# Performance work log

Measured on AMD Instinct MI355X. Metric: run time of the kernel, lower is better.

## Reference

```python
import jax, jax.numpy as jnp
import numpy as np

N = 30000      # particles
E = 300000     # directed edges
H = 128        # hidden size
L = 10         # GNN layers
EMB = 16       # particle-type embedding size
T = 5          # velocity history window
NTYPES = 9
RADIUS = 0.05
OUT = 2
NODE_IN = 2 * T + 4 + EMB  # 30


def _mlp_ln(x, W1, b1, W2, b2, W3, b3, g, be):
    # Linear-ReLU-Linear-ReLU-Linear-LayerNorm (matches node/edge encoders and GraphNet blocks)
    h = jax.nn.relu(x @ W1 + b1)
    h = jax.nn.relu(h @ W2 + b2)
    h = h @ W3 + b3
    mu = jnp.mean(h, axis=-1, keepdims=True)
    var = jnp.mean((h - mu) ** 2, axis=-1, keepdims=True)
    return (h - mu) * jax.lax.rsqrt(var + 1e-5) * g + be


def setup_inputs() -> dict:
    key = jax.random.key(0)
    ks = iter(jax.random.split(key, 48))
    nx = lambda: next(ks)
    inp = {}
    inp["vel"] = jax.random.normal(nx(), (N, T, 2), jnp.float32) * 0.01
    inp["pos"] = jax.random.uniform(nx(), (N, 2), dtype=jnp.float32)
    inp["bounds"] = jnp.array([[0.0, 1.0], [0.0, 1.0]], jnp.float32)  # [dim, (lo,hi)]
    inp["tgt_pos"] = jax.random.uniform(nx(), (N, 2), dtype=jnp.float32)
    inp["particle_type"] = jax.random.randint(nx(), (N,), 0, NTYPES, jnp.int32)
    inp["nonk_mask"] = jax.random.randint(nx(), (N,), 0, 2, jnp.int32)
    inp["senders"] = jax.random.randint(nx(), (E,), 0, N, jnp.int32)
    inp["receivers"] = jax.random.randint(nx(), (E,), 0, N, jnp.int32)
    inp["emb"] = jax.random.normal(nx(), (NTYPES, EMB), jnp.float32) * 0.1

    def mlp_p(pre, din, lead=()):
        w = lambda i, o: jax.random.normal(nx(), lead + (i, o), jnp.float32) / np.sqrt(i)
        inp[pre + "_W1"] = w(din, H); inp[pre + "_b1"] = jnp.zeros(lead + (H,), jnp.float32)
        inp[pre + "_W2"] = w(H, H);   inp[pre + "_b2"] = jnp.zeros(lead + (H,), jnp.float32)
        inp[pre + "_W3"] = w(H, H);   inp[pre + "_b3"] = jnp.zeros(lead + (H,), jnp.float32)
        inp[pre + "_g"] = jnp.ones(lead + (H,), jnp.float32)
        inp[pre + "_be"] = jnp.zeros(lead + (H,), jnp.float32)

    mlp_p("ne", NODE_IN)          # node encoder
    mlp_p("ee", 3)                # edge encoder
    mlp_p("ge", 3 * H, (L,))      # per-layer edge-update MLPs
    mlp_p("gn", 2 * H, (L,))      # per-layer node-update MLPs
    inp["de_W1"] = jax.random.normal(nx(), (H, H), jnp.float32) / np.sqrt(H)
    inp["de_b1"] = jnp.zeros((H,), jnp.float32)
    inp["de_W2"] = jax.random.normal(nx(), (H, H), jnp.float32) / np.sqrt(H)
    inp["de_b2"] = jnp.zeros((H,), jnp.float32)
    inp["de_W3"] = jax.random.normal(nx(), (H, OUT), jnp.float32) / np.sqrt(H)
    inp["de_b3"] = jnp.zeros((OUT,), jnp.float32)
    return inp


def reference(vel, pos, bounds, tgt_pos, particle_type, nonk_mask, senders, receivers, emb,
              ne_W1, ne_b1, ne_W2, ne_b2, ne_W3, ne_b3, ne_g, ne_be,
              ee_W1, ee_b1, ee_W2, ee_b2, ee_W3, ee_b3, ee_g, ee_be,
              ge_W1, ge_b1, ge_W2, ge_b2, ge_W3, ge_b3, ge_g, ge_be,
              gn_W1, gn_b1, gn_W2, gn_b2, gn_W3, gn_b3, gn_g, gn_be,
              de_W1, de_b1, de_W2, de_b2, de_W3, de_b3):
    n = pos.shape[0]
    # --- construct node features ---
    vels = vel.reshape(n, -1)                                   # [N, T*2]
    dtw = jnp.concatenate([pos - bounds[:, 0], bounds[:, 1] - pos], axis=1)
    dtw = jnp.clip(dtw / RADIUS, -1.0, 1.0)                     # [N, 4]
    type_emb = emb[particle_type]                               # [N, EMB] gather
    node_attr = jnp.concatenate([vels, dtw, type_emb], axis=1)  # [N, 30]
    # --- construct edge features (senders/receivers precomputed; KD-tree is CPU-side) ---
    dist_vec = (pos[senders] - pos[receivers]) / RADIUS         # [E, 2]
    dist = jnp.linalg.norm(dist_vec, axis=1, keepdims=True)     # [E, 1]
    edge_attr = jnp.concatenate([dist_vec, dist], axis=1)       # [E, 3]
    # --- encode ---
    nodes = _mlp_ln(node_attr, ne_W1, ne_b1, ne_W2, ne_b2, ne_W3, ne_b3, ne_g, ne_be)
    edges = _mlp_ln(edge_attr, ee_W1, ee_b1, ee_W2, ee_b2, ee_W3, ee_b3, ee_g, ee_be)
    # --- process: L message-passing layers with residuals ---
    for l in range(ge_W1.shape[0]):
        e_in = jnp.concatenate([edges, nodes[senders], nodes[receivers]], axis=1)  # [E, 3H]
        edges = edges + _mlp_ln(e_in, ge_W1[l], ge_b1[l], ge_W2[l], ge_b2[l], ge_W3[l], ge_b3[l], ge_g[l], ge_be[l])
        agg = jax.ops.segment_sum(edges, receivers, num_segments=n)               # [N, H] scatter-add
        n_in = jnp.concatenate([nodes, agg], axis=1)                              # [N, 2H]
        nodes = nodes + _mlp_ln(n_in, gn_W1[l], gn_b1[l], gn_W2[l], gn_b2[l], gn_W3[l], gn_b3[l], gn_g[l], gn_be[l])
    # --- decode ---
    h = jax.nn.relu(nodes @ de_W1 + de_b1)
    h = jax.nn.relu(h @ de_W2 + de_b2)
    pred_acc = h @ de_W3 + de_b3                                 # [N, 2]
    # --- Euler integration step (out_size == 2 branch) ---
    pred_pos = pos + vel[:, -1, :] + pred_acc
    pred_pos = jnp.where(nonk_mask[:, None].astype(bool), pred_pos, tgt_pos)
    return pred_acc[:, None, :], pred_pos[:, None, :]
```

## Files before the change

kernel.cpp:

```cpp
#include <hip/hip_runtime.h>
#include <hip/hip_bf16.h>

typedef __hip_bfloat16 bf16;
typedef unsigned short u16;
typedef unsigned int u32;
typedef __attribute__((ext_vector_type(8))) short short8;
typedef __attribute__((ext_vector_type(4))) float f32x4;
typedef __attribute__((ext_vector_type(4))) unsigned int u32x4;

#define NPART 30000
#define NEDGE 300000
#define HD 128
#define NLAYER 10
#define NFLOAT_ARRAYS 43
#define NMAT 66

__device__ __forceinline__ bool detect_bf16(const unsigned short* braw) {
    return braw[1] == 0x3F80u;
}

__device__ __forceinline__ u16 f2b(float f) {
    u32 u = __float_as_uint(f);
    u += 0x7FFFu + ((u >> 16) & 1u);
    return (u16)(u >> 16);
}
__device__ __forceinline__ u32 pack2(float a, float b) {
    return (u32)f2b(a) | ((u32)f2b(b) << 16);
}
__device__ __forceinline__ float b2flo(u32 u) { return __uint_as_float(u << 16); }
__device__ __forceinline__ float b2fhi(u32 u) { return __uint_as_float(u & 0xFFFF0000u); }

__device__ __forceinline__ u32x4 ntl4(const u16* p) {
    return __builtin_nontemporal_load((const u32x4*)p);
}
__device__ __forceinline__ void nts4(const u32x4 v, u16* p) {
    __builtin_nontemporal_store(v, (u32x4*)p);
}
__device__ __forceinline__ f32x4 ntlf4(const float* p) {
    return __builtin_nontemporal_load((const f32x4*)p);
}
__device__ __forceinline__ void ntsf4(const f32x4 v, float* p) {
    __builtin_nontemporal_store(v, (f32x4*)p);
}

struct ConvArgs {
    const void* src[NFLOAT_ARRAYS];
    int n[NFLOAT_ARRAYS];
    int off[NFLOAT_ARRAYS];
};

__global__ __launch_bounds__(256)
void k_convert(ConvArgs a, float* __restrict__ dst, const unsigned short* __restrict__ braw)
{
    const bool isb = detect_bf16(braw);
    const int aid = blockIdx.y;
    const int n = a.n[aid];
    float* o = dst + a.off[aid];
    const int stride = gridDim.x * 256;
    int i = blockIdx.x * 256 + threadIdx.x;
    if (isb) {
        const unsigned short* s = (const unsigned short*)a.src[aid];
        for (; i < n; i += stride) {
            const unsigned int u = ((unsigned int)s[i]) << 16;
            o[i] = __uint_as_float(u);
        }
    } else {
        const float* s = (const float*)a.src[aid];
        for (; i < n; i += stride) o[i] = s[i];
    }
}

__global__ __launch_bounds__(256)
void k_hist(const int* __restrict__ rcv, int* __restrict__ counts)
{
    const int e = blockIdx.x * 256 + threadIdx.x;
    if (e < NEDGE) atomicAdd(&counts[rcv[e]], 1);
}

__global__ __launch_bounds__(1024)
void k_scan(const int* __restrict__ counts, int* __restrict__ row_ptr, int* __restrict__ cursor)
{
    __shared__ int part[1024];
    const int t = threadIdx.x;
    const int base = t * 32;
    int local[32];
    int s = 0;
#pragma unroll
    for (int k = 0; k < 32; k++) {
        const int idx = base + k;
        const int v = (idx < NPART) ? counts[idx] : 0;
        local[k] = s;
        s += v;
    }
    part[t] = s;
    __syncthreads();
    for (int off = 1; off < 1024; off <<= 1) {
        const int v = (t >= off) ? part[t - off] : 0;
        __syncthreads();
        part[t] += v;
        __syncthreads();
    }
    const int excl = (t == 0) ? 0 : part[t - 1];
#pragma unroll
    for (int k = 0; k < 32; k++) {
        const int idx = base + k;
        if (idx < NPART) {
            const int rp = excl + local[k];
            row_ptr[idx] = rp;
            cursor[idx] = rp;
        }
    }
    if (t == 0) row_ptr[NPART] = NEDGE;
}

__global__ __launch_bounds__(256)
void k_scatter(const int* __restrict__ snd, const int* __restrict__ rcv,
               int* __restrict__ cursor, int* __restrict__ snd_s, int* __restrict__ rcv_s)
{
    const int e = blockIdx.x * 256 + threadIdx.x;
    if (e < NEDGE) {
        const int r = rcv[e];
        const int p = atomicAdd(&cursor[r], 1);
        snd_s[p] = snd[e];
        rcv_s[p] = r;
    }
}

struct PackArgs {
    int src_off[NMAT];
    int dst_off[NMAT];
    int K[NMAT];
    int nks[NMAT];
};

__global__ __launch_bounds__(256)
void k_pack(const float* __restrict__ cw, u16* __restrict__ wpk, PackArgs pa)
{
    const int mid = blockIdx.y;
    const int nks = pa.nks[mid];
    const int total = nks * 4096;
    const int d = blockIdx.x * 256 + threadIdx.x;
    if (d >= total) return;
    const int j = d & 7, l = (d >> 3) & 63, t = d >> 9;
    const int ks = t % nks, mt = t / nks;
    const int hid = mt * 16 + (l & 15);
    const int k = ks * 32 + (l >> 4) * 8 + j;
    const float v = (k < pa.K[mid]) ? cw[pa.src_off[mid] + k * HD + hid] : 0.0f;
    wpk[pa.dst_off[mid] + d] = f2b(v);
}

template<int NKS, int XROW>
__device__ __forceinline__ void gemm16(const u16* __restrict__ Wp,
                                       const float* __restrict__ Bias,
                                       const u16* __restrict__ x,
                                       f32x4 acc[4][2],
                                       const int wm, const int wn,
                                       const int l15, const int lg, const int lane)
{
#pragma unroll
    for (int mt = 0; mt < 4; mt++) {
        const f32x4 bv = *(const f32x4*)(Bias + wm * 64 + mt * 16 + lg * 4);
        acc[mt][0] = bv;
        acc[mt][1] = bv;
    }
    const u16* xr0 = x + (wn * 32 + l15) * XROW + lg * 8;
    const u16* xr1 = xr0 + 16 * XROW;
    const u16* wp = Wp + (wm * 4 * NKS) * 512 + lane * 8;
#pragma unroll
    for (int ks = 0; ks < NKS; ks++) {
        const short8 b0 = *(const short8*)(xr0 + ks * 32);
        const short8 b1 = *(const short8*)(xr1 + ks * 32);
#pragma unroll
        for (int mt = 0; mt < 4; mt++) {
            const short8 a = *(const short8*)(wp + (mt * NKS + ks) * 512);
            acc[mt][0] = __builtin_amdgcn_mfma_f32_16x16x32_bf16(a, b0, acc[mt][0], 0, 0, 0);
            acc[mt][1] = __builtin_amdgcn_mfma_f32_16x16x32_bf16(a, b1, acc[mt][1], 0, 0, 0);
        }
    }
}

__device__ __forceinline__ void store_h(u16* __restrict__ h, const f32x4 acc[4][2],
                                        const int wm, const int wn, const int l15, const int lg)
{
#pragma unroll
    for (int nt = 0; nt < 2; nt++) {
        const int e = wn * 32 + nt * 16 + l15;
#pragma unroll
        for (int mt = 0; mt < 4; mt++) {
            const int hid = wm * 64 + mt * 16 + lg * 4;
            const f32x4 v = acc[mt][nt];
            const u32 lo = pack2(fmaxf(v[0], 0.0f), fmaxf(v[1], 0.0f));
            const u32 hi = pack2(fmaxf(v[2], 0.0f), fmaxf(v[3], 0.0f));
            *(uint2*)(h + e * 136 + hid) = make_uint2(lo, hi);
        }
    }
}

template<int NKS1, int XROW>
__device__ __forceinline__ void mlp_mfma(const u16* __restrict__ xs,
    u16* __restrict__ h1, u16* __restrict__ h2,
    float (*red)[2][2][16][2],
    const u16* __restrict__ W1p, const float* __restrict__ B1,
    const u16* __restrict__ W2p, const float* __restrict__ B2,
    const u16* __restrict__ W3p, const float* __restrict__ B3,
    const float* __restrict__ g, const float* __restrict__ be,
    float outv[4][2][4],
    const int wm, const int wn, const int l15, const int lg, const int lane)
{
    f32x4 acc[4][2];
    gemm16<NKS1, XROW>(W1p, B1, xs, acc, wm, wn, l15, lg, lane);
    __syncthreads();
    store_h(h1, acc, wm, wn, l15, lg);
    __syncthreads();
    gemm16<4, 136>(W2p, B2, h1, acc, wm, wn, l15, lg, lane);
    store_h(h2, acc, wm, wn, l15, lg);
    __syncthreads();
    gemm16<4, 136>(W3p, B3, h2, acc, wm, wn, l15, lg, lane);
    float ps[2], pss[2];
#pragma unroll
    for (int nt = 0; nt < 2; nt++) {
        float s = 0.0f, ss = 0.0f;
#pragma unroll
        for (int mt = 0; mt < 4; mt++) {
#pragma unroll
            for (int r = 0; r < 4; r++) {
                const float v = acc[mt][nt][r];
                s += v; ss += v * v;
            }
        }
        s += __shfl_xor(s, 16); ss += __shfl_xor(ss, 16);
        s += __shfl_xor(s, 32); ss += __shfl_xor(ss, 32);
        ps[nt] = s; pss[nt] = ss;
    }
    if (lane < 16) {
#pragma unroll
        for (int nt = 0; nt < 2; nt++) {
            red[wm][wn][nt][l15][0] = ps[nt];
            red[wm][wn][nt][l15][1] = pss[nt];
        }
    }
    __syncthreads();
#pragma unroll
    for (int nt = 0; nt < 2; nt++) {
        const float S  = red[0][wn][nt][l15][0] + red[1][wn][nt][l15][0];
        const float SS = red[0][wn][nt][l15][1] + red[1][wn][nt][l15][1];
        const float mu  = S * (1.0f / 128.0f);
        const float var = SS * (1.0f / 128.0f) - mu * mu;
        const float inv = rsqrtf(var + 1e-5f);
#pragma unroll
        for (int mt = 0; mt < 4; mt++) {
            const int hid = wm * 64 + mt * 16 + lg * 4;
            const f32x4 gv  = *(const f32x4*)(g + hid);
            const f32x4 bev = *(const f32x4*)(be + hid);
#pragma unroll
            for (int r = 0; r < 4; r++)
                outv[mt][nt][r] = (acc[mt][nt][r] - mu) * inv * gv[r] + bev[r];
        }
    }
}

__device__ __forceinline__ float nfeat(int i, int k,
    const float* __restrict__ vel, const float* __restrict__ pos,
    const float* __restrict__ bounds, const int* __restrict__ ptype,
    const float* __restrict__ emb)
{
    if (k < 10) return vel[i * 10 + k];
    if (k < 14) {
        const int q = k - 10;
        float sub;
        if (q < 2) sub = pos[i * 2 + q] - bounds[q * 2 + 0];
        else       sub = bounds[(q - 2) * 2 + 1] - pos[i * 2 + (q - 2)];
        const float dv = sub * 20.0f;
        return fminf(fmaxf(dv, -1.0f), 1.0f);
    }
    if (k < 30) return emb[ptype[i] * 16 + (k - 14)];
    return 0.0f;
}

__global__ __launch_bounds__(256)
void k_node_enc_m(const float* __restrict__ vel, const float* __restrict__ pos,
                  const float* __restrict__ bounds, const int* __restrict__ ptype,
                  const float* __restrict__ emb,
                  const u16* __restrict__ W1p, const float* __restrict__ B1,
                  const u16* __restrict__ W2p, const float* __restrict__ B2,
                  const u16* __restrict__ W3p, const float* __restrict__ B3,
                  const float* __restrict__ g, const float* __restrict__ be,
                  u16* __restrict__ nodes_bf)
{
    __shared__ __align__(16) u16 lds[17408];
    __shared__ float red[2][2][2][16][2];
    const int tid = threadIdx.x;
    const int i0 = blockIdx.x * 64;
    for (int idx = tid; idx < 1024; idx += 256) {
        const int m = idx >> 4, kk = idx & 15;
        const int i = i0 + m;
        float f0 = 0.0f, f1 = 0.0f;
        if (i < NPART) {
            f0 = nfeat(i, kk * 2 + 0, vel, pos, bounds, ptype, emb);
            f1 = nfeat(i, kk * 2 + 1, vel, pos, bounds, ptype, emb);
        }
        *(u32*)(lds + m * 40 + kk * 2) = pack2(f0, f1);
    }
    __syncthreads();
    const int lane = tid & 63, wv = tid >> 6;
    const int wm = wv >> 1, wn = wv & 1, l15 = lane & 15, lg = lane >> 4;
    float outv[4][2][4];
    mlp_mfma<1, 40>(lds, lds, lds + 8704, red, W1p, B1, W2p, B2, W3p, B3, g, be,
                    outv, wm, wn, l15, lg, lane);
#pragma unroll
    for (int nt = 0; nt < 2; nt++) {
        const int i = i0 + wn * 32 + nt * 16 + l15;
        if (i < NPART) {
#pragma unroll
            for (int mt = 0; mt < 4; mt++) {
                const int hid = wm * 64 + mt * 16 + lg * 4;
                *(uint2*)(nodes_bf + (size_t)i * HD + hid) =
                    make_uint2(pack2(outv[mt][nt][0], outv[mt][nt][1]),
                               pack2(outv[mt][nt][2], outv[mt][nt][3]));
            }
        }
    }
}

__global__ __launch_bounds__(256)
void k_edge_enc_m(const float* __restrict__ pos, const int* __restrict__ snd_s,
                  const int* __restrict__ rcv_s,
                  const u16* __restrict__ W1p, const float* __restrict__ B1,
                  const u16* __restrict__ W2p, const float* __restrict__ B2,
                  const u16* __restrict__ W3p, const float* __restrict__ B3,
                  const float* __restrict__ g, const float* __restrict__ be,
                  u16* __restrict__ edges_bf)
{
    __shared__ __align__(16) u16 lds[17408];
    __shared__ float red[2][2][2][16][2];
    const int tid = threadIdx.x;
    const int e0 = blockIdx.x * 64;
    for (int idx = tid; idx < 1024; idx += 256) {
        const int m = idx >> 4, kk = idx & 15;
        const int e = min(e0 + m, NEDGE - 1);
        u32 w = 0;
        if (kk < 2) {
            const int s = snd_s[e], r = rcv_s[e];
            const float dx = (pos[s * 2 + 0] - pos[r * 2 + 0]) * 20.0f;
            const float dy = (pos[s * 2 + 1] - pos[r * 2 + 1]) * 20.0f;
            if (kk == 0) w = pack2(dx, dy);
            else         w = pack2(sqrtf(dx * dx + dy * dy), 0.0f);
        }
        *(u32*)(lds + m * 40 + kk * 2) = w;
    }
    __syncthreads();
    const int lane = tid & 63, wv = tid >> 6;
    const int wm = wv >> 1, wn = wv & 1, l15 = lane & 15, lg = lane >> 4;
    float outv[4][2][4];
    mlp_mfma<1, 40>(lds, lds, lds + 8704, red, W1p, B1, W2p, B2, W3p, B3, g, be,
                    outv, wm, wn, l15, lg, lane);
#pragma unroll
    for (int nt = 0; nt < 2; nt++) {
        const int e = e0 + wn * 32 + nt * 16 + l15;
        if (e < NEDGE) {
#pragma unroll
            for (int mt = 0; mt < 4; mt++) {
                const int hid = wm * 64 + mt * 16 + lg * 4;
                *(uint2*)(edges_bf + (size_t)e * HD + hid) =
                    make_uint2(pack2(outv[mt][nt][0], outv[mt][nt][1]),
                               pack2(outv[mt][nt][2], outv[mt][nt][3]));
            }
        }
    }
}

__device__ __forceinline__ void egemm_seg32(const u16* __restrict__ Wp,
                                            const u16* __restrict__ x,
                                            f32x4 acc[2][2], const int ks0,
                                            const int wm,
                                            const int l15, const int lg, const int lane)
{
    const u16* xr0 = x + l15 * 136 + lg * 8;
    const u16* xr1 = xr0 + 16 * 136;
#pragma unroll
    for (int ks = 0; ks < 4; ks++) {
        const short8 b0 = *(const short8*)(xr0 + ks * 32);
        const short8 b1 = *(const short8*)(xr1 + ks * 32);
#pragma unroll
        for (int mt = 0; mt < 2; mt++) {
            const short8 a = *(const short8*)(Wp + (((wm * 2 + mt) * 12 + ks0 + ks) * 64 + lane) * 8);
            acc[mt][0] = __builtin_amdgcn_mfma_f32_16x16x32_bf16(a, b0, acc[mt][0], 0, 0, 0);
            acc[mt][1] = __builtin_amdgcn_mfma_f32_16x16x32_bf16(a, b1, acc[mt][1], 0, 0, 0);
        }
    }
}

__device__ __forceinline__ void egemm_h32(const u16* __restrict__ Wp,
                                          const float* __restrict__ Bias,
                                          const u16* __restrict__ x,
                                          f32x4 acc[2][2],
                                          const int wm,
                                          const int l15, const int lg, const int lane)
{
#pragma unroll
    for (int mt = 0; mt < 2; mt++) {
        const f32x4 bv = *(const f32x4*)(Bias + wm * 32 + mt * 16 + lg * 4);
        acc[mt][0] = bv;
        acc[mt][1] = bv;
    }
    const u16* xr0 = x + l15 * 136 + lg * 8;
    const u16* xr1 = xr0 + 16 * 136;
#pragma unroll
    for (int ks = 0; ks < 4; ks++) {
        const short8 b0 = *(const short8*)(xr0 + ks * 32);
        const short8 b1 = *(const short8*)(xr1 + ks * 32);
#pragma unroll
        for (int mt = 0; mt < 2; mt++) {
            const short8 a = *(const short8*)(Wp + (((wm * 2 + mt) * 4 + ks) * 64 + lane) * 8);
            acc[mt][0] = __builtin_amdgcn_mfma_f32_16x16x32_bf16(a, b0, acc[mt][0], 0, 0, 0);
            acc[mt][1] = __builtin_amdgcn_mfma_f32_16x16x32_bf16(a, b1, acc[mt][1], 0, 0, 0);
        }
    }
}

__device__ __forceinline__ void estore_h32(u16* __restrict__ h, const f32x4 acc[2][2],
                                           const int wm, const int l15, const int lg)
{
#pragma unroll
    for (int nt = 0; nt < 2; nt++) {
        const int row = nt * 16 + l15;
#pragma unroll
        for (int mt = 0; mt < 2; mt++) {
            const int hid = wm * 32 + mt * 16 + lg * 4;
            const f32x4 v = acc[mt][nt];
            const u32 lo = pack2(fmaxf(v[0], 0.0f), fmaxf(v[1], 0.0f));
            const u32 hi = pack2(fmaxf(v[2], 0.0f), fmaxf(v[3], 0.0f));
            *(uint2*)(h + row * 136 + hid) = make_uint2(lo, hi);
        }
    }
}

__global__ __launch_bounds__(256, 8)
void k_edge_layer_m(const u16* __restrict__ nodes_bf, u16* __restrict__ edges_bf,
                    float* __restrict__ agg, float* __restrict__ bnd,
                    const int* __restrict__ snd_s, const int* __restrict__ rcv_s,
                    const u16* __restrict__ W1p, const float* __restrict__ B1,
                    const u16* __restrict__ W2p, const float* __restrict__ B2,
                    const u16* __restrict__ W3p, const float* __restrict__ B3,
                    const float* __restrict__ g, const float* __restrict__ be)
{
    __shared__ __align__(16) u16 sb[2 * 4352];
    __shared__ float red[4][2][16][2];
    __shared__ int rblk[34];
    u16* b0 = sb;
    u16* b1 = sb + 4352;
    float* fout = (float*)sb;

    const int tid = threadIdx.x;
    const int e0 = blockIdx.x * 32;
    const int lane = tid & 63, wm = tid >> 6;
    const int l15 = lane & 15, lg = lane >> 4;

    if (tid < 32)       rblk[tid] = rcv_s[e0 + tid];
    else if (tid == 32) rblk[32] = (e0 > 0) ? rcv_s[e0 - 1] : -2;
    else if (tid == 33) rblk[33] = (e0 + 32 < NEDGE) ? rcv_s[e0 + 32] : -2;

    u32x4 e_old[2];
#pragma unroll
    for (int t = 0; t < 2; t++) {
        const int idx = tid + t * 256;
        const int m = idx >> 4, q = idx & 15;
        e_old[t] = ntl4(edges_bf + (size_t)(e0 + m) * HD + q * 8);
        *(u32x4*)(b0 + m * 136 + q * 8) = e_old[t];
    }
    u32x4 st[2];
#pragma unroll
    for (int t = 0; t < 2; t++) {
        const int idx = tid + t * 256;
        const int m = idx >> 4, q = idx & 15;
        st[t] = *(const u32x4*)(nodes_bf + (size_t)snd_s[e0 + m] * HD + q * 8);
    }
    __syncthreads();

    f32x4 acc[2][2];
#pragma unroll
    for (int mt = 0; mt < 2; mt++) {
        const f32x4 bv = *(const f32x4*)(B1 + wm * 32 + mt * 16 + lg * 4);
        acc[mt][0] = bv;
        acc[mt][1] = bv;
    }
    __builtin_amdgcn_s_setprio(1);
    egemm_seg32(W1p, b0, acc, 0, wm, l15, lg, lane);
    __builtin_amdgcn_s_setprio(0);
#pragma unroll
    for (int t = 0; t < 2; t++) {
        const int idx = tid + t * 256;
        const int m = idx >> 4, q = idx & 15;
        *(u32x4*)(b1 + m * 136 + q * 8) = st[t];
    }
#pragma unroll
    for (int t = 0; t < 2; t++) {
        const int idx = tid + t * 256;
        const int m = idx >> 4, q = idx & 15;
        st[t] = *(const u32x4*)(nodes_bf + (size_t)rcv_s[e0 + m] * HD + q * 8);
    }
    __syncthreads();

    __builtin_amdgcn_s_setprio(1);
    egemm_seg32(W1p, b1, acc, 4, wm, l15, lg, lane);
    __builtin_amdgcn_s_setprio(0);
#pragma unroll
    for (int t = 0; t < 2; t++) {
        const int idx = tid + t * 256;
        const int m = idx >> 4, q = idx & 15;
        *(u32x4*)(b0 + m * 136 + q * 8) = st[t];
    }
    __syncthreads();

    __builtin_amdgcn_s_setprio(1);
    egemm_seg32(W1p, b0, acc, 8, wm, l15, lg, lane);
    __builtin_amdgcn_s_setprio(0);
    estore_h32(b1, acc, wm, l15, lg);
    __syncthreads();

    __builtin_amdgcn_s_setprio(1);
    egemm_h32(W2p, B2, b1, acc, wm, l15, lg, lane);
    __builtin_amdgcn_s_setprio(0);
    estore_h32(b0, acc, wm, l15, lg);
    __syncthreads();

    __builtin_amdgcn_s_setprio(1);
    egemm_h32(W3p, B3, b0, acc, wm, l15, lg, lane);
    __builtin_amdgcn_s_setprio(0);

    float ps[2], pss[2];
#pragma unroll
    for (int nt = 0; nt < 2; nt++) {
        float s = 0.0f, ss = 0.0f;
#pragma unroll
        for (int mt = 0; mt < 2; mt++) {
#pragma unroll
            for (int r = 0; r < 4; r++) {
                const float v = acc[mt][nt][r];
                s += v; ss += v * v;
            }
        }
        s += __shfl_xor(s, 16); ss += __shfl_xor(ss, 16);
        s += __shfl_xor(s, 32); ss += __shfl_xor(ss, 32);
        ps[nt] = s; pss[nt] = ss;
    }
    if (lane < 16) {
#pragma unroll
        for (int nt = 0; nt < 2; nt++) {
            red[wm][nt][l15][0] = ps[nt];
            red[wm][nt][l15][1] = pss[nt];
        }
    }
    __syncthreads();

#pragma unroll
    for (int nt = 0; nt < 2; nt++) {
        const float S  = red[0][nt][l15][0] + red[1][nt][l15][0]
                       + red[2][nt][l15][0] + red[3][nt][l15][0];
        const float SS = red[0][nt][l15][1] + red[1][nt][l15][1]
                       + red[2][nt][l15][1] + red[3][nt][l15][1];
        const float mu  = S * (1.0f / 128.0f);
        const float var = SS * (1.0f / 128.0f) - mu * mu;
        const float inv = rsqrtf(var + 1e-5f);
        const int row = nt * 16 + l15;
#pragma unroll
        for (int mt = 0; mt < 2; mt++) {
            const int hid = wm * 32 + mt * 16 + lg * 4;
            const f32x4 gv  = *(const f32x4*)(g + hid);
            const f32x4 bev = *(const f32x4*)(be + hid);
            f32x4 o;
#pragma unroll
            for (int r = 0; r < 4; r++)
                o[r] = (acc[mt][nt][r] - mu) * inv * gv[r] + bev[r];
            *(f32x4*)(fout + row * 132 + hid) = o;
        }
    }
    __syncthreads();

#pragma unroll
    for (int t = 0; t < 2; t++) {
        const int idx = tid + t * 256;
        const int m = idx >> 4, q = idx & 15;
        float4 lo = *(const float4*)(fout + m * 132 + q * 8);
        float4 hi = *(const float4*)(fout + m * 132 + q * 8 + 4);
        const u32x4 o = e_old[t];
        lo.x += b2flo(o.x); lo.y += b2fhi(o.x);
        lo.z += b2flo(o.y); lo.w += b2fhi(o.y);
        hi.x += b2flo(o.z); hi.y += b2fhi(o.z);
        hi.z += b2flo(o.w); hi.w += b2fhi(o.w);
        *(float4*)(fout + m * 132 + q * 8) = lo;
        *(float4*)(fout + m * 132 + q * 8 + 4) = hi;
        u32x4 nv;
        nv.x = pack2(lo.x, lo.y); nv.y = pack2(lo.z, lo.w);
        nv.z = pack2(hi.x, hi.y); nv.w = pack2(hi.z, hi.w);
        nts4(nv, edges_bf + (size_t)(e0 + m) * HD + q * 8);
    }
    __syncthreads();

    const int c = tid & 31;
    for (int ms = (tid >> 5); ms < 32; ms += 8) {
        const int rs = rblk[ms];
        if (ms > 0 && rblk[ms - 1] == rs) continue;
        int me = ms + 1;
        while (me < 32 && rblk[me] == rs) me++;
        f32x4 s = {0.0f, 0.0f, 0.0f, 0.0f};
        for (int m = ms; m < me; m++) {
            const float4 v = *(const float4*)(fout + m * 132 + c * 4);
            s.x += v.x; s.y += v.y; s.z += v.z; s.w += v.w;
        }
        const bool extb = (ms == 0 && rblk[32] == rs);
        const bool extf = (me == 32 && rblk[33] == rs);
        float* ap;
        if (!extb && !extf) ap = agg + (size_t)rs * HD + c * 4;
        else ap = bnd + ((size_t)blockIdx.x * 2 + (extb ? 0 : 1)) * HD + c * 4;
        ntsf4(s, ap);
    }
}

__global__ __launch_bounds__(256)
void k_node_layer_m(u16* __restrict__ nodes_bf,
                    const float* __restrict__ agg, const float* __restrict__ bnd,
                    const int* __restrict__ row_ptr,
                    const u16* __restrict__ W1p, const float* __restrict__ B1,
                    const u16* __restrict__ W2p, const float* __restrict__ B2,
                    const u16* __restrict__ W3p, const float* __restrict__ B3,
                    const float* __restrict__ g, const float* __restrict__ be)
{
    __shared__ __align__(16) u16 lds[17408];
    __shared__ float red[2][2][2][16][2];
    __shared__ int rp[65];
    const int tid = threadIdx.x;
    const int i0 = blockIdx.x * 64;
    if (tid < 65) rp[tid] = row_ptr[min(i0 + tid, NPART)];
    __syncthreads();
    for (int idx = tid; idx < 1024; idx += 256) {
        const int m = idx >> 4, q = idx & 15;
        const int i = min(i0 + m, NPART - 1);
        *(u32x4*)(lds + m * 264 + q * 8) =
            *(const u32x4*)(nodes_bf + (size_t)i * HD + q * 8);
    }
    for (int idx = tid; idx < 1024; idx += 256) {
        const int m = idx >> 4, q = idx & 15;
        const int i = i0 + m;
        f32x4 a = {0.0f, 0.0f, 0.0f, 0.0f};
        f32x4 b = {0.0f, 0.0f, 0.0f, 0.0f};
        if (i < NPART) {
            const int p0 = rp[m], p1 = rp[m + 1];
            if (p1 > p0) {
                const int b0 = p0 >> 5, b1 = (p1 - 1) >> 5;
                if (b0 == b1) {
                    const float* src = agg + (size_t)i * HD + q * 8;
                    a = ntlf4(src);
                    b = ntlf4(src + 4);
                } else {
                    const float* s1 = bnd + ((size_t)b0 * 2 + 1) * HD + q * 8;
                    a = ntlf4(s1);
                    b = ntlf4(s1 + 4);
                    for (int bb = b0 + 1; bb <= b1; bb++) {
                        const float* s0 = bnd + ((size_t)bb * 2 + 0) * HD + q * 8;
                        const f32x4 xa = ntlf4(s0);
                        const f32x4 xb = ntlf4(s0 + 4);
                        a += xa;
                        b += xb;
                    }
                }
            }
        }
        *(u32x4*)(lds + m * 264 + 128 + q * 8) = (u32x4){
            pack2(a.x, a.y), pack2(a.z, a.w), pack2(b.x, b.y), pack2(b.z, b.w)};
    }
    __syncthreads();
    const int lane = tid & 63, wv = tid >> 6;
    const int wm = wv >> 1, wn = wv & 1, l15 = lane & 15, lg = lane >> 4;
    float outv[4][2][4];
    mlp_mfma<8, 264>(lds, lds, lds + 8704, red, W1p, B1, W2p, B2, W3p, B3, g, be,
                     outv, wm, wn, l15, lg, lane);
#pragma unroll
    for (int nt = 0; nt < 2; nt++) {
        const int i = i0 + wn * 32 + nt * 16 + l15;
        if (i < NPART) {
            u16* np = nodes_bf + (size_t)i * HD;
#pragma unroll
            for (int mt = 0; mt < 4; mt++) {
                const int hid = wm * 64 + mt * 16 + lg * 4;
                const uint2 ob = *(const uint2*)(np + hid);
                float4 nv;
                nv.x = b2flo(ob.x) + outv[mt][nt][0];
                nv.y = b2fhi(ob.x) + outv[mt][nt][1];
                nv.z = b2flo(ob.y) + outv[mt][nt][2];
                nv.w = b2fhi(ob.y) + outv[mt][nt][3];
                *(uint2*)(np + hid) = make_uint2(pack2(nv.x, nv.y), pack2(nv.z, nv.w));
            }
        }
    }
}

template<int K, int S>
__device__ __forceinline__ void gemv(const float* __restrict__ in,
                                     const float* __restrict__ W,
                                     const float* __restrict__ B,
                                     float acc[8])
{
    const int j = threadIdx.x;
    const float bb = B[j];
#pragma unroll
    for (int m = 0; m < 8; m++) acc[m] = bb;
    constexpr int K4 = (K / 4) * 4;
    for (int k = 0; k < K4; k += 4) {
        const float w0 = W[(k + 0) * HD + j];
        const float w1 = W[(k + 1) * HD + j];
        const float w2 = W[(k + 2) * HD + j];
        const float w3 = W[(k + 3) * HD + j];
#pragma unroll
        for (int m = 0; m < 8; m++) {
            const float4 x = *(const float4*)(in + m * S + k);
            float a = acc[m];
            a = fmaf(x.x, w0, a);
            a = fmaf(x.y, w1, a);
            a = fmaf(x.z, w2, a);
            a = fmaf(x.w, w3, a);
            acc[m] = a;
        }
    }
#pragma unroll
    for (int k = K4; k < K; k++) {
        const float w = W[k * HD + j];
#pragma unroll
        for (int m = 0; m < 8; m++) acc[m] = fmaf(in[m * S + k], w, acc[m]);
    }
}

__global__ __launch_bounds__(128)
void k_decoder(const u16* __restrict__ nodes_bf,
               const float* W1, const float* B1, const float* W2, const float* B2,
               const float* W3, const float* B3,
               const float* __restrict__ vel, const float* __restrict__ pos,
               const float* __restrict__ tgt, const int* __restrict__ nonk,
               const unsigned short* __restrict__ braw, void* __restrict__ d_out)
{
    __shared__ __align__(16) float xs[8 * HD];
    __shared__ __align__(16) float h1[8 * HD];
    __shared__ __align__(16) float h2[8 * HD];
    const int j = threadIdx.x;
    const int i0 = blockIdx.x * 8;
    float acc[8];
    for (int idx = j; idx < 512; idx += 128) {
        const int m = idx >> 6, q = idx & 63;
        const u32 w = *(const u32*)(nodes_bf + (size_t)(i0 + m) * HD + q * 2);
        xs[m * HD + q * 2]     = b2flo(w);
        xs[m * HD + q * 2 + 1] = b2fhi(w);
    }
    __syncthreads();
    gemv<HD, HD>(xs, W1, B1, acc);
#pragma unroll
    for (int m = 0; m < 8; m++) h1[m * HD + j] = fmaxf(acc[m], 0.0f);
    __syncthreads();
    gemv<HD, HD>(h1, W2, B2, acc);
#pragma unroll
    for (int m = 0; m < 8; m++) h2[m * HD + j] = fmaxf(acc[m], 0.0f);
    __syncthreads();
    if (j < 16) {
        const int m = j >> 1, d = j & 1, i = i0 + m;
        float a = B3[d];
        for (int k = 0; k < HD; k++) a = fmaf(h2[m * HD + k], W3[k * 2 + d], a);
        float pp = pos[i * 2 + d] + vel[i * 10 + 8 + d] + a;
        if (nonk[i] == 0) pp = tgt[i * 2 + d];
        if (detect_bf16(braw)) {
            bf16* o = (bf16*)d_out;
            o[i * 2 + d] = __float2bfloat16(a);
            o[2 * NPART + i * 2 + d] = __float2bfloat16(pp);
        } else {
            float* o = (float*)d_out;
            o[i * 2 + d] = a;
            o[2 * NPART + i * 2 + d] = pp;
        }
    }
}

extern "C" void kernel_launch(void* const* d_in, const int* in_sizes, int n_in,
                              void* d_out, int out_size, void* d_ws, size_t ws_size,
                              hipStream_t stream)
{
    const int* ptype = (const int*)d_in[4];
    const int* nonk  = (const int*)d_in[5];
    const int* snd   = (const int*)d_in[6];
    const int* rcv   = (const int*)d_in[7];
    const unsigned short* braw = (const unsigned short*)d_in[2];

    int fmap[NFLOAT_ARRAYS];
    {
        int c = 0;
        fmap[c++] = 0; fmap[c++] = 1; fmap[c++] = 2; fmap[c++] = 3; fmap[c++] = 8;
        for (int i = 9; i <= 46; i++) fmap[c++] = i;
    }
    ConvArgs ca;
    const float* fp[47];
    float* cw = (float*)d_ws;
    int off = 0;
    for (int i = 0; i < NFLOAT_ARRAYS; i++) {
        ca.src[i] = d_in[fmap[i]];
        ca.n[i]   = in_sizes[fmap[i]];
        ca.off[i] = off;
        fp[fmap[i]] = cw + off;
        off += in_sizes[fmap[i]];
    }
    const int EB32 = NEDGE / 32;
    float* agg   = cw + ((off + 3) & ~3);
    float* bnd   = agg + (size_t)NPART * HD;
    u16* edges_bf = (u16*)(bnd + (size_t)EB32 * 2 * HD);
    u16* nodes_bf = edges_bf + (size_t)NEDGE * HD;
    u16* wpk = nodes_bf + (size_t)NPART * HD;

    PackArgs pa;
    int dst = 0, c = 0;
    int pk[NMAT];
    auto addm = [&](long srcoff, int K) {
        const int nk = (K + 31) / 32;
        pa.src_off[c] = (int)srcoff;
        pa.K[c] = K;
        pa.nks[c] = nk;
        pa.dst_off[c] = dst;
        pk[c] = dst;
        dst += nk * 4096;
        c++;
    };
    addm(fp[9]  - cw, 30);  addm(fp[11] - cw, 128); addm(fp[13] - cw, 128);
    addm(fp[17] - cw, 3);   addm(fp[19] - cw, 128); addm(fp[21] - cw, 128);
    for (int l = 0; l < NLAYER; l++) {
        addm(fp[25] - cw + (long)l * 384 * HD, 384);
        addm(fp[27] - cw + (long)l * HD * HD, 128);
        addm(fp[29] - cw + (long)l * HD * HD, 128);
    }
    for (int l = 0; l < NLAYER; l++) {
        addm(fp[33] - cw + (long)l * 256 * HD, 256);
        addm(fp[35] - cw + (long)l * HD * HD, 128);
        addm(fp[37] - cw + (long)l * HD * HD, 128);
    }

    int* ip = (int*)(wpk + ((dst + 7) & ~7));
    int* row_ptr = ip;            ip += NPART + 8;
    int* cursor  = ip;            ip += NPART;
    int* counts  = ip;            ip += NPART;
    int* snd_s   = ip;            ip += NEDGE;
    int* rcv_s   = ip;

    const int EBL = (NEDGE + 255) / 256;

    k_convert<<<dim3(64, NFLOAT_ARRAYS), 256, 0, stream>>>(ca, cw, braw);
    hipMemsetAsync(counts, 0, (size_t)NPART * sizeof(int), stream);
    k_hist<<<EBL, 256, 0, stream>>>(rcv, counts);
    k_scan<<<1, 1024, 0, stream>>>(counts, row_ptr, cursor);
    k_scatter<<<EBL, 256, 0, stream>>>(snd, rcv, cursor, snd_s, rcv_s);
    k_pack<<<dim3(192, NMAT), 256, 0, stream>>>(cw, wpk, pa);

    const int NB = (NPART + 63) / 64;
    const int EB = (NEDGE + 63) / 64;

    k_node_enc_m<<<NB, 256, 0, stream>>>(fp[0], fp[1], fp[2], ptype, fp[8],
        wpk + pk[0], fp[10], wpk + pk[1], fp[12], wpk + pk[2], fp[14],
        fp[15], fp[16], nodes_bf);
    k_edge_enc_m<<<EB, 256, 0, stream>>>(fp[1], snd_s, rcv_s,
        wpk + pk[3], fp[18], wpk + pk[4], fp[20], wpk + pk[5], fp[22],
        fp[23], fp[24], edges_bf);

    for (int l = 0; l < NLAYER; l++) {
        k_edge_layer_m<<<EB32, 256, 0, stream>>>(nodes_bf, edges_bf, agg, bnd, snd_s, rcv_s,
            wpk + pk[6 + 3 * l],  fp[26] + (size_t)l * HD,
            wpk + pk[7 + 3 * l],  fp[28] + (size_t)l * HD,
            wpk + pk[8 + 3 * l],  fp[30] + (size_t)l * HD,
            fp[31] + (size_t)l * HD, fp[32] + (size_t)l * HD);
        k_node_layer_m<<<NB, 256, 0, stream>>>(nodes_bf, agg, bnd, row_ptr,
            wpk + pk[36 + 3 * l], fp[34] + (size_t)l * HD,
            wpk + pk[37 + 3 * l], fp[36] + (size_t)l * HD,
            wpk + pk[38 + 3 * l], fp[38] + (size_t)l * HD,
            fp[39] + (size_t)l * HD, fp[40] + (size_t)l * HD);
    }

    k_decoder<<<NPART / 8, 128, 0, stream>>>(nodes_bf,
        fp[41], fp[42], fp[43], fp[44], fp[45], fp[46],
        fp[0], fp[1], fp[3], nonk, braw, d_out);
}
```

Before: 1.835 ms.

## Shrink node-layer tiles to 32 rows, remap edge blocks per XCD, use intrinsic bf16 convert

Rewrites the node-layer kernel to process 32 nodes per block using the same 4-wave edge-style MFMA helpers, with an explicit LayerNorm reduction, doubling the block count for better occupancy and load balance. The edge-layer kernel remaps block IDs so that consecutive edge tiles land on the same XCD, which should improve L2 locality for the sorted receivers. The bf16 rounding helper now uses the library conversion intrinsic. These changes raise launch count and weight reloads per node, and the intrinsic conversion may handle NaN differently.

Result: slower. 1.904 ms (+3.7%).

```diff
diff --git a/kernel.cpp b/kernel.cpp
--- a/kernel.cpp
+++ b/kernel.cpp
@@ -20,9 +20,10 @@
 }
 
 __device__ __forceinline__ u16 f2b(float f) {
-    u32 u = __float_as_uint(f);
-    u += 0x7FFFu + ((u >> 16) & 1u);
-    return (u16)(u >> 16);
+    const bf16 h = __float2bfloat16(f);
+    u16 u;
+    __builtin_memcpy(&u, &h, sizeof(u));
+    return u;
 }
 __device__ __forceinline__ u32 pack2(float a, float b) {
     return (u32)f2b(a) | ((u32)f2b(b) << 16);
@@ -418,6 +419,34 @@
     }
 }
 
+__device__ __forceinline__ void egemm_n1(const u16* __restrict__ Wp,
+                                         const float* __restrict__ Bias,
+                                         const u16* __restrict__ x,
+                                         f32x4 acc[2][2],
+                                         const int wm,
+                                         const int l15, const int lg, const int lane)
+{
+#pragma unroll
+    for (int mt = 0; mt < 2; mt++) {
+        const f32x4 bv = *(const f32x4*)(Bias + wm * 32 + mt * 16 + lg * 4);
+        acc[mt][0] = bv;
+        acc[mt][1] = bv;
+    }
+    const u16* xr0 = x + l15 * 264 + lg * 8;
+    const u16* xr1 = xr0 + 16 * 264;
+#pragma unroll
+    for (int ks = 0; ks < 8; ks++) {
+        const short8 b0 = *(const short8*)(xr0 + ks * 32);
+        const short8 b1 = *(const short8*)(xr1 + ks * 32);
+#pragma unroll
+        for (int mt = 0; mt < 2; mt++) {
+            const short8 a = *(const short8*)(Wp + (((wm * 2 + mt) * 8 + ks) * 64 + lane) * 8);
+            acc[mt][0] = __builtin_amdgcn_mfma_f32_16x16x32_bf16(a, b0, acc[mt][0], 0, 0, 0);
+            acc[mt][1] = __builtin_amdgcn_mfma_f32_16x16x32_bf16(a, b1, acc[mt][1], 0, 0, 0);
+        }
+    }
+}
+
 __device__ __forceinline__ void estore_h32(u16* __restrict__ h, const f32x4 acc[2][2],
                                            const int wm, const int l15, const int lg)
 {
@@ -452,7 +481,11 @@
     float* fout = (float*)sb;
 
     const int tid = threadIdx.x;
-    const int e0 = blockIdx.x * 32;
+    const int nwg = NEDGE / 32;
+    const int qq = nwg >> 3, rr = nwg & 7;
+    const int xcd = blockIdx.x & 7, sub = blockIdx.x >> 3;
+    const int tile = (xcd < rr ? xcd * (qq + 1) : rr * (qq + 1) + (xcd - rr) * qq) + sub;
+    const int e0 = tile * 32;
     const int lane = tid & 63, wm = tid >> 6;
     const int l15 = lane & 15, lg = lane >> 4;
 
@@ -612,7 +645,7 @@
         const bool extf = (me == 32 && rblk[33] == rs);
         float* ap;
         if (!extb && !extf) ap = agg + (size_t)rs * HD + c * 4;
-        else ap = bnd + ((size_t)blockIdx.x * 2 + (extb ? 0 : 1)) * HD + c * 4;
+        else ap = bnd + ((size_t)tile * 2 + (extb ? 0 : 1)) * HD + c * 4;
         ntsf4(s, ap);
     }
 }
@@ -626,20 +659,27 @@
                     const u16* __restrict__ W3p, const float* __restrict__ B3,
                     const float* __restrict__ g, const float* __restrict__ be)
 {
-    __shared__ __align__(16) u16 lds[17408];
-    __shared__ float red[2][2][2][16][2];
-    __shared__ int rp[65];
+    __shared__ __align__(16) u16 xs[32 * 264];
+    __shared__ __align__(16) u16 hb[32 * 136];
+    __shared__ float red[4][2][16][2];
+    __shared__ int rp[33];
     const int tid = threadIdx.x;
-    const int i0 = blockIdx.x * 64;
-    if (tid < 65) rp[tid] = row_ptr[min(i0 + tid, NPART)];
-    __syncthreads();
-    for (int idx = tid; idx < 1024; idx += 256) {
+    const int i0 = blockIdx.x * 32;
+    const int lane = tid & 63, wm = tid >> 6;
+    const int l15 = lane & 15, lg = lane >> 4;
+    if (tid < 33) rp[tid] = row_ptr[min(i0 + tid, NPART)];
+    __syncthreads();
+#pragma unroll
+    for (int t = 0; t < 2; t++) {
+        const int idx = tid + t * 256;
         const int m = idx >> 4, q = idx & 15;
         const int i = min(i0 + m, NPART - 1);
-        *(u32x4*)(lds + m * 264 + q * 8) =
+        *(u32x4*)(xs + m * 264 + q * 8) =
             *(const u32x4*)(nodes_bf + (size_t)i * HD + q * 8);
     }
-    for (int idx = tid; idx < 1024; idx += 256) {
+#pragma unroll
+    for (int t = 0; t < 2; t++) {
+        const int idx = tid + t * 256;
         const int m = idx >> 4, q = idx & 15;
         const int i = i0 + m;
         f32x4 a = {0.0f, 0.0f, 0.0f, 0.0f};
@@ -647,48 +687,91 @@
         if (i < NPART) {
             const int p0 = rp[m], p1 = rp[m + 1];
             if (p1 > p0) {
-                const int b0 = p0 >> 5, b1 = (p1 - 1) >> 5;
-                if (b0 == b1) {
+                const int b0i = p0 >> 5, b1i = (p1 - 1) >> 5;
+                if (b0i == b1i) {
                     const float* src = agg + (size_t)i * HD + q * 8;
                     a = ntlf4(src);
                     b = ntlf4(src + 4);
                 } else {
-                    const float* s1 = bnd + ((size_t)b0 * 2 + 1) * HD + q * 8;
+                    const float* s1 = bnd + ((size_t)b0i * 2 + 1) * HD + q * 8;
                     a = ntlf4(s1);
                     b = ntlf4(s1 + 4);
-                    for (int bb = b0 + 1; bb <= b1; bb++) {
+                    for (int bb = b0i + 1; bb <= b1i; bb++) {
                         const float* s0 = bnd + ((size_t)bb * 2 + 0) * HD + q * 8;
-                        const f32x4 xa = ntlf4(s0);
-                        const f32x4 xb = ntlf4(s0 + 4);
-                        a += xa;
-                        b += xb;
+                        a += ntlf4(s0);
+                        b += ntlf4(s0 + 4);
                     }
                 }
             }
         }
-        *(u32x4*)(lds + m * 264 + 128 + q * 8) = (u32x4){
+        *(u32x4*)(xs + m * 264 + 128 + q * 8) = (u32x4){
             pack2(a.x, a.y), pack2(a.z, a.w), pack2(b.x, b.y), pack2(b.z, b.w)};
     }
     __syncthreads();
-    const int lane = tid & 63, wv = tid >> 6;
-    const int wm = wv >> 1, wn = wv & 1, l15 = lane & 15, lg = lane >> 4;
-    float outv[4][2][4];
-    mlp_mfma<8, 264>(lds, lds, lds + 8704, red, W1p, B1, W2p, B2, W3p, B3, g, be,
-                     outv, wm, wn, l15, lg, lane);
+
+    f32x4 acc[2][2];
+    __builtin_amdgcn_s_setprio(1);
+    egemm_n1(W1p, B1, xs, acc, wm, l15, lg, lane);
+    __builtin_amdgcn_s_setprio(0);
+    estore_h32(hb, acc, wm, l15, lg);
+    __syncthreads();
+    __builtin_amdgcn_s_setprio(1);
+    egemm_h32(W2p, B2, hb, acc, wm, l15, lg, lane);
+    __builtin_amdgcn_s_setprio(0);
+    estore_h32(xs, acc, wm, l15, lg);
+    __syncthreads();
+    __builtin_amdgcn_s_setprio(1);
+    egemm_h32(W3p, B3, xs, acc, wm, l15, lg, lane);
+    __builtin_amdgcn_s_setprio(0);
+
+    float ps[2], pss[2];
 #pragma unroll
     for (int nt = 0; nt < 2; nt++) {
-        const int i = i0 + wn * 32 + nt * 16 + l15;
+        float s = 0.0f, ss = 0.0f;
+#pragma unroll
+        for (int mt = 0; mt < 2; mt++) {
+#pragma unroll
+            for (int r = 0; r < 4; r++) {
+                const float v = acc[mt][nt][r];
+                s += v; ss += v * v;
+            }
+        }
+        s += __shfl_xor(s, 16); ss += __shfl_xor(ss, 16);
+        s += __shfl_xor(s, 32); ss += __shfl_xor(ss, 32);
+        ps[nt] = s; pss[nt] = ss;
+    }
+    if (lane < 16) {
+#pragma unroll
+        for (int nt = 0; nt < 2; nt++) {
+            red[wm][nt][l15][0] = ps[nt];
+            red[wm][nt][l15][1] = pss[nt];
+        }
+    }
+    __syncthreads();
+
+#pragma unroll
+    for (int nt = 0; nt < 2; nt++) {
+        const float S  = red[0][nt][l15][0] + red[1][nt][l15][0]
+                       + red[2][nt][l15][0] + red[3][nt][l15][0];
+        const float SS = red[0][nt][l15][1] + red[1][nt][l15][1]
+                       + red[2][nt][l15][1] + red[3][nt][l15][1];
+        const float mu  = S * (1.0f / 128.0f);
+        const float var = SS * (1.0f / 128.0f) - mu * mu;
+        const float inv = rsqrtf(var + 1e-5f);
+        const int i = i0 + nt * 16 + l15;
         if (i < NPART) {
             u16* np = nodes_bf + (size_t)i * HD;
 #pragma unroll
-            for (int mt = 0; mt < 4; mt++) {
-                const int hid = wm * 64 + mt * 16 + lg * 4;
+            for (int mt = 0; mt < 2; mt++) {
+                const int hid = wm * 32 + mt * 16 + lg * 4;
+                const f32x4 gv  = *(const f32x4*)(g + hid);
+                const f32x4 bev = *(const f32x4*)(be + hid);
                 const uint2 ob = *(const uint2*)(np + hid);
                 float4 nv;
-                nv.x = b2flo(ob.x) + outv[mt][nt][0];
-                nv.y = b2fhi(ob.x) + outv[mt][nt][1];
-                nv.z = b2flo(ob.y) + outv[mt][nt][2];
-                nv.w = b2fhi(ob.y) + outv[mt][nt][3];
+                nv.x = b2flo(ob.x) + (acc[mt][nt][0] - mu) * inv * gv[0] + bev[0];
+                nv.y = b2fhi(ob.x) + (acc[mt][nt][1] - mu) * inv * gv[1] + bev[1];
+                nv.z = b2flo(ob.y) + (acc[mt][nt][2] - mu) * inv * gv[2] + bev[2];
+                nv.w = b2fhi(ob.y) + (acc[mt][nt][3] - mu) * inv * gv[3] + bev[3];
                 *(uint2*)(np + hid) = make_uint2(pack2(nv.x, nv.y), pack2(nv.z, nv.w));
             }
         }
@@ -854,6 +937,7 @@
     k_pack<<<dim3(192, NMAT), 256, 0, stream>>>(cw, wpk, pa);
 
     const int NB = (NPART + 63) / 64;
+    const int NB32 = (NPART + 31) / 32;
     const int EB = (NEDGE + 63) / 64;
 
     k_node_enc_m<<<NB, 256, 0, stream>>>(fp[0], fp[1], fp[2], ptype, fp[8],
@@ -869,7 +953,7 @@
             wpk + pk[7 + 3 * l],  fp[28] + (size_t)l * HD,
             wpk + pk[8 + 3 * l],  fp[30] + (size_t)l * HD,
             fp[31] + (size_t)l * HD, fp[32] + (size_t)l * HD);
-        k_node_layer_m<<<NB, 256, 0, stream>>>(nodes_bf, agg, bnd, row_ptr,
+        k_node_layer_m<<<NB32, 256, 0, stream>>>(nodes_bf, agg, bnd, row_ptr,
             wpk + pk[36 + 3 * l], fp[34] + (size_t)l * HD,
             wpk + pk[37 + 3 * l], fp[36] + (size_t)l * HD,
             wpk + pk[38 + 3 * l], fp[38] + (size_t)l * HD,
```
